# Kernel optimization log

Hardware: AMD Instinct MI355X
Metric: run time of the kernel (lower is better)

Reference implementation:

```python
import math
import jax, jax.numpy as jnp
import numpy as np

DIM = 1024
N_HEADS = 16
N_KV_HEADS = 4
HEAD_DIM = 64
WINDOW = 512
EPS = 1e-6
B, S = 2, 2048

def _alibi_slopes(n_heads):
    def pow2(n):
        r = 2.0 ** (-8.0 / n)
        return np.array([r ** (i + 1) for i in range(n)], dtype=np.float32)
    if math.log2(n_heads).is_integer():
        return pow2(n_heads)
    m = 2 ** math.floor(math.log2(n_heads))
    return np.concatenate([pow2(m), pow2(2 * m)[::2][: n_heads - m]])

def _rmsnorm(x, w, eps=EPS):
    var = jnp.mean(x * x, axis=-1, keepdims=True)
    return x * jax.lax.rsqrt(var + eps) * w

def setup_inputs() -> dict:
    key = jax.random.key(0)
    ks = jax.random.split(key, 8)
    x = jax.random.normal(ks[0], (B, S, DIM), dtype=jnp.float32)
    wq = 0.02 * jax.random.normal(ks[1], (N_HEADS * HEAD_DIM, DIM), dtype=jnp.float32)
    wk = 0.02 * jax.random.normal(ks[2], (N_KV_HEADS * HEAD_DIM, DIM), dtype=jnp.float32)
    wv = 0.02 * jax.random.normal(ks[3], (N_KV_HEADS * HEAD_DIM, DIM), dtype=jnp.float32)
    wo = 0.02 * jax.random.normal(ks[4], (DIM, N_HEADS * HEAD_DIM), dtype=jnp.float32)
    q_norm_w = jnp.ones((N_HEADS * HEAD_DIM,), dtype=jnp.float32)
    k_norm_w = jnp.ones((N_KV_HEADS * HEAD_DIM,), dtype=jnp.float32)
    return {"x": x, "wq": wq, "wk": wk, "wv": wv, "wo": wo,
            "q_norm_w": q_norm_w, "k_norm_w": k_norm_w}

def reference(x, wq, wk, wv, wo, q_norm_w, k_norm_w):
    bsz, seqlen, _ = x.shape
    repeats = N_HEADS // N_KV_HEADS
    xq = _rmsnorm(x @ wq.T, q_norm_w)
    xk = _rmsnorm(x @ wk.T, k_norm_w)
    xv = x @ wv.T
    # [b, h, s, d]
    q = xq.reshape(bsz, seqlen, N_HEADS, HEAD_DIM).transpose(0, 2, 1, 3)
    k = xk.reshape(bsz, seqlen, N_KV_HEADS, HEAD_DIM).transpose(0, 2, 1, 3)
    v = xv.reshape(bsz, seqlen, N_KV_HEADS, HEAD_DIM).transpose(0, 2, 1, 3)
    k = jnp.repeat(k, repeats, axis=1)
    v = jnp.repeat(v, repeats, axis=1)
    pos = jnp.arange(seqlen)
    rel = pos[None, :] - pos[:, None]  # [s_q, s_k], key - query
    slopes = jnp.asarray(_alibi_slopes(N_HEADS))
    bias = slopes[:, None, None] * rel[None].astype(x.dtype)  # [h, s, s]
    masked = (rel > 0) | (rel < -WINDOW)  # causal + sliding window
    bias = jnp.where(masked[None], -jnp.inf, bias)
    scale = 1.0 / math.sqrt(HEAD_DIM)
    scores = jnp.einsum('bhqd,bhkd->bhqk', q, k) * scale + bias[None]
    probs = jax.nn.softmax(scores, axis=-1)
    y = jnp.einsum('bhqk,bhkd->bhqd', probs, v)
    y = y.transpose(0, 2, 1, 3).reshape(bsz, seqlen, N_HEADS * HEAD_DIM)
    return y @ wo.T
```

## Files before the change

kernel.cpp:

```cpp
#include <hip/hip_runtime.h>

typedef unsigned short u16;
typedef unsigned int u32;

typedef __bf16 bf16x8 __attribute__((ext_vector_type(8)));
typedef float f32x4 __attribute__((ext_vector_type(4)));

__device__ __forceinline__ u16 f2bf(float f) {
  u32 u = __builtin_bit_cast(u32, f);
  u32 r = (u + 0x7fffu + ((u >> 16) & 1u)) >> 16;
  return (u16)r;
}
__device__ __forceinline__ float bf2f(u16 v) {
  u32 u = (u32)v << 16;
  return __builtin_bit_cast(float, u);
}

__global__ __launch_bounds__(256)
void cvt_all_kernel(const float* __restrict__ x, const float* __restrict__ wq,
                    const float* __restrict__ wk, const float* __restrict__ wv,
                    const float* __restrict__ wo, u16* __restrict__ x_bf,
                    u16* __restrict__ wcat_bf, u16* __restrict__ wo_bf) {
  int t = blockIdx.x * 256 + threadIdx.x;
  const float* src;
  u16* dst;
  if (t < 1048576) {
    src = x; dst = x_bf;
  } else if (t < 1310720) {
    src = wq; dst = wcat_bf; t -= 1048576;
  } else if (t < 1376256) {
    src = wk; dst = wcat_bf + 1048576; t -= 1310720;
  } else if (t < 1441792) {
    src = wv; dst = wcat_bf + 1310720; t -= 1376256;
  } else {
    src = wo; dst = wo_bf; t -= 1441792;
  }
  const int i = t * 4;
  float4 v = *(const float4*)(src + i);
  uint2 p;
  p.x = (u32)f2bf(v.x) | ((u32)f2bf(v.y) << 16);
  p.y = (u32)f2bf(v.z) | ((u32)f2bf(v.w) << 16);
  *(uint2*)(dst + i) = p;
}

template <typename OutT>
__global__ __launch_bounds__(256)
void gemm_bt_kernel(const u16* __restrict__ A, const u16* __restrict__ B,
                    OutT* __restrict__ C, int M, int N, int K) {
  __shared__ u16 As[64 * 32];
  __shared__ u16 Bs[128 * 32];
  const int tid = threadIdx.x;
  const int lane = tid & 63;
  const int wave = tid >> 6;
  const int wm = (wave >> 1) * 32;
  const int wn = (wave & 1) * 64;
  const int l15 = lane & 15;
  const int qk = (lane >> 4) * 8;
  const size_t bm = (size_t)blockIdx.y * 64;
  const size_t bn = (size_t)blockIdx.x * 128;

  f32x4 acc[2][4];
#pragma unroll
  for (int i = 0; i < 2; ++i)
#pragma unroll
    for (int j = 0; j < 4; ++j) acc[i][j] = f32x4{0.f, 0.f, 0.f, 0.f};

  const int r0 = tid >> 2;
  const int c0 = (tid & 3) * 8;
  const u16* Ab = A + (bm + r0) * (size_t)K + c0;
  const u16* Bb = B + (bn + r0) * (size_t)K + c0;

  uint4 ar = *(const uint4*)(Ab);
  uint4 br0 = *(const uint4*)(Bb);
  uint4 br1 = *(const uint4*)(Bb + (size_t)64 * K);

  for (int k0 = 0; k0 < K; k0 += 32) {
    __syncthreads();
    *(uint4*)(&As[tid * 8]) = ar;
    *(uint4*)(&Bs[tid * 8]) = br0;
    *(uint4*)(&Bs[tid * 8 + 2048]) = br1;
    __syncthreads();
    const int kn = (k0 + 32 < K) ? k0 + 32 : 0;
    ar = *(const uint4*)(Ab + kn);
    br0 = *(const uint4*)(Bb + kn);
    br1 = *(const uint4*)(Bb + (size_t)64 * K + kn);
    bf16x8 af[2], bfr[4];
#pragma unroll
    for (int i = 0; i < 2; ++i)
      af[i] = *(const bf16x8*)(&As[(wm + i * 16 + l15) * 32 + qk]);
#pragma unroll
    for (int j = 0; j < 4; ++j)
      bfr[j] = *(const bf16x8*)(&Bs[(wn + j * 16 + l15) * 32 + qk]);
#pragma unroll
    for (int i = 0; i < 2; ++i)
#pragma unroll
      for (int j = 0; j < 4; ++j)
        acc[i][j] = __builtin_amdgcn_mfma_f32_16x16x32_bf16(af[i], bfr[j], acc[i][j], 0, 0, 0);
  }

  const int rq = (lane >> 4) * 4;
#pragma unroll
  for (int i = 0; i < 2; ++i) {
#pragma unroll
    for (int r = 0; r < 4; ++r) {
      OutT* crow = C + (bm + wm + i * 16 + rq + r) * (size_t)N + bn + wn + l15;
#pragma unroll
      for (int j = 0; j < 4; ++j) {
        if constexpr (sizeof(OutT) == 2)
          crow[j * 16] = f2bf(acc[i][j][r]);
        else
          crow[j * 16] = acc[i][j][r];
      }
    }
  }
}

__global__ __launch_bounds__(256)
void norm_vtrans_kernel(u16* __restrict__ qkv, const float* __restrict__ qw,
                        const float* __restrict__ kw, u16* __restrict__ vt) {
  __shared__ u16 shmem[64 * 72];
  const int bid = blockIdx.x;
  const int tid = threadIdx.x;
  if (bid < 4096) {
    float* red = (float*)shmem;
    u16* row = qkv + (size_t)bid * 1536;
    uint2 pk = *(const uint2*)(row + tid * 4);
    float v0 = bf2f((u16)pk.x), v1 = bf2f((u16)(pk.x >> 16));
    float v2 = bf2f((u16)pk.y), v3 = bf2f((u16)(pk.y >> 16));
    float ss = v0 * v0 + v1 * v1 + v2 * v2 + v3 * v3;
#pragma unroll
    for (int off = 32; off > 0; off >>= 1) ss += __shfl_down(ss, off);
    if ((tid & 63) == 0) red[tid >> 6] = ss;
    __syncthreads();
    float tot = red[0] + red[1] + red[2] + red[3];
    float rn = rsqrtf(tot * (1.0f / 1024.0f) + 1e-6f);
    float4 w = *(const float4*)(qw + tid * 4);
    uint2 po;
    po.x = (u32)f2bf(v0 * rn * w.x) | ((u32)f2bf(v1 * rn * w.y) << 16);
    po.y = (u32)f2bf(v2 * rn * w.z) | ((u32)f2bf(v3 * rn * w.w) << 16);
    *(uint2*)(row + tid * 4) = po;
    if (tid < 64) {
      uint2 kp = *(const uint2*)(row + 1024 + tid * 4);
      float k0 = bf2f((u16)kp.x), k1 = bf2f((u16)(kp.x >> 16));
      float k2 = bf2f((u16)kp.y), k3 = bf2f((u16)(kp.y >> 16));
      float sk = k0 * k0 + k1 * k1 + k2 * k2 + k3 * k3;
#pragma unroll
      for (int off = 32; off > 0; off >>= 1) sk += __shfl_down(sk, off);
      float tk = __shfl(sk, 0);
      float rk = rsqrtf(tk * (1.0f / 256.0f) + 1e-6f);
      float4 w2 = *(const float4*)(kw + tid * 4);
      uint2 ko;
      ko.x = (u32)f2bf(k0 * rk * w2.x) | ((u32)f2bf(k1 * rk * w2.y) << 16);
      ko.y = (u32)f2bf(k2 * rk * w2.z) | ((u32)f2bf(k3 * rk * w2.w) << 16);
      *(uint2*)(row + 1024 + tid * 4) = ko;
    }
  } else {
    const int e = bid - 4096;
    const int t0 = (e & 31) * 64, kvh = (e >> 5) & 3, b = e >> 7;
    u16(*tile)[72] = (u16(*)[72])shmem;
    const int r = tid >> 2, c16 = (tid & 3) * 16;
    const u16* src = qkv + (size_t)(b * 2048 + t0 + r) * 1536 + 1280 + kvh * 64 + c16;
    *(uint4*)&tile[r][c16] = *(const uint4*)src;
    *(uint4*)&tile[r][c16 + 8] = *(const uint4*)(src + 8);
    __syncthreads();
    const int d = tid >> 2, t16 = (tid & 3) * 16;
    u16 o[16];
#pragma unroll
    for (int j = 0; j < 16; ++j) o[j] = tile[t16 + j][d];
    u16* dst = vt + (size_t)((b * 4 + kvh) * 64 + d) * 2048 + t0 + t16;
    *(uint4*)dst = *(uint4*)&o[0];
    *(uint4*)(dst + 8) = *(uint4*)&o[8];
  }
}

__global__ __launch_bounds__(256)
void attn_kernel(const u16* __restrict__ qkvbf, const u16* __restrict__ vt,
                 u16* __restrict__ ybf) {
  __shared__ u16 Ks[64 * 72];
  __shared__ u16 Vts[64 * 72];
  __shared__ u16 Ps[64 * 72];
  const int qt = blockIdx.x, h = blockIdx.y, b = blockIdx.z;
  const int kvh = h >> 2, q0 = qt * 64;
  const int tid = threadIdx.x, lane = tid & 63, w = tid >> 6;
  const int l15 = lane & 15, quad = lane >> 4;

  const u16* qrow = qkvbf + (size_t)(b * 2048 + q0 + w * 16 + l15) * 1536 + h * 64 + quad * 8;
  const bf16x8 qf0 = *(const bf16x8*)qrow;
  const bf16x8 qf1 = *(const bf16x8*)(qrow + 32);

  const int sr = tid >> 2, sc = (tid & 3) * 16;
  const u16* kbase = qkvbf + (size_t)(b * 2048 + sr) * 1536 + 1024 + kvh * 64 + sc;
  const u16* vbase = vt + (size_t)((b * 4 + kvh) * 64 + sr) * 2048 + sc;

  f32x4 O[4];
#pragma unroll
  for (int jd = 0; jd < 4; ++jd) O[jd] = f32x4{0.f, 0.f, 0.f, 0.f};
  float m_i = -1e30f, l_i = 0.f;
  const float LOG2E = 1.44269504f;
  const float sc2 = 0.125f * LOG2E;
  const float slope2 = exp2f(-0.5f * (float)(h + 1)) * LOG2E;
  const int c_lo = (q0 >= 512) ? (q0 - 512) : 0;
  const int myq = q0 + w * 16 + l15;
  const int myq_lo = q0 + w * 16;

  uint4 kr0, kr1, vr0, vr1;
  {
    const u16* kp = kbase + (size_t)c_lo * 1536;
    const u16* vp = vbase + c_lo;
    kr0 = *(const uint4*)kp;  kr1 = *(const uint4*)(kp + 8);
    vr0 = *(const uint4*)vp;  vr1 = *(const uint4*)(vp + 8);
  }

  for (int c = c_lo; c <= q0; c += 64) {
    __syncthreads();
    *(uint4*)&Ks[sr * 72 + sc] = kr0;
    *(uint4*)&Ks[sr * 72 + sc + 8] = kr1;
    *(uint4*)&Vts[sr * 72 + sc] = vr0;
    *(uint4*)&Vts[sr * 72 + sc + 8] = vr1;
    __syncthreads();
    {
      const int cn = (c + 64 <= q0) ? c + 64 : c_lo;
      const u16* kp = kbase + (size_t)cn * 1536;
      const u16* vp = vbase + cn;
      kr0 = *(const uint4*)kp;  kr1 = *(const uint4*)(kp + 8);
      vr0 = *(const uint4*)vp;  vr1 = *(const uint4*)(vp + 8);
    }

    f32x4 st[4];
#pragma unroll
    for (int i = 0; i < 4; ++i) {
      bf16x8 a0 = *(const bf16x8*)&Ks[(i * 16 + l15) * 72 + quad * 8];
      bf16x8 a1 = *(const bf16x8*)&Ks[(i * 16 + l15) * 72 + 32 + quad * 8];
      f32x4 z = f32x4{0.f, 0.f, 0.f, 0.f};
      z = __builtin_amdgcn_mfma_f32_16x16x32_bf16(a0, qf0, z, 0, 0, 0);
      st[i] = __builtin_amdgcn_mfma_f32_16x16x32_bf16(a1, qf1, z, 0, 0, 0);
    }

    float sv[4][4];
    float rm = -1e30f;
    const bool interior = (c + 63 <= myq_lo) && (c + 512 >= myq_lo + 15);
    if (interior) {
#pragma unroll
      for (int i = 0; i < 4; ++i)
#pragma unroll
        for (int r = 0; r < 4; ++r) {
          const int key = c + i * 16 + quad * 4 + r;
          float val = st[i][r] * sc2 + slope2 * (float)(key - myq);
          sv[i][r] = val;
          rm = fmaxf(rm, val);
        }
    } else {
#pragma unroll
      for (int i = 0; i < 4; ++i)
#pragma unroll
        for (int r = 0; r < 4; ++r) {
          const int key = c + i * 16 + quad * 4 + r;
          const int rel = key - myq;
          float val = (rel > 0 || rel < -512) ? -1e30f
                                              : st[i][r] * sc2 + slope2 * (float)rel;
          sv[i][r] = val;
          rm = fmaxf(rm, val);
        }
    }
    rm = fmaxf(rm, __shfl_xor(rm, 16));
    rm = fmaxf(rm, __shfl_xor(rm, 32));
    const float mn = fmaxf(m_i, rm);
    const float alpha = exp2f(m_i - mn);
    float ls = 0.f;
#pragma unroll
    for (int i = 0; i < 4; ++i) {
      float p0 = exp2f(sv[i][0] - mn);
      float p1 = exp2f(sv[i][1] - mn);
      float p2 = exp2f(sv[i][2] - mn);
      float p3 = exp2f(sv[i][3] - mn);
      ls += (p0 + p1) + (p2 + p3);
      uint2 pw;
      pw.x = (u32)f2bf(p0) | ((u32)f2bf(p1) << 16);
      pw.y = (u32)f2bf(p2) | ((u32)f2bf(p3) << 16);
      *(uint2*)&Ps[(w * 16 + l15) * 72 + i * 16 + quad * 4] = pw;
    }
    ls += __shfl_xor(ls, 16);
    ls += __shfl_xor(ls, 32);
    l_i = l_i * alpha + ls;
    m_i = mn;

    float ar[4];
#pragma unroll
    for (int r = 0; r < 4; ++r) ar[r] = __shfl(alpha, quad * 4 + r);
#pragma unroll
    for (int jd = 0; jd < 4; ++jd)
#pragma unroll
      for (int r = 0; r < 4; ++r) O[jd][r] *= ar[r];

    bf16x8 pf0 = *(const bf16x8*)&Ps[(w * 16 + l15) * 72 + quad * 8];
    bf16x8 pf1 = *(const bf16x8*)&Ps[(w * 16 + l15) * 72 + 32 + quad * 8];
#pragma unroll
    for (int jd = 0; jd < 4; ++jd) {
      bf16x8 v0 = *(const bf16x8*)&Vts[(jd * 16 + l15) * 72 + quad * 8];
      bf16x8 v1 = *(const bf16x8*)&Vts[(jd * 16 + l15) * 72 + 32 + quad * 8];
      O[jd] = __builtin_amdgcn_mfma_f32_16x16x32_bf16(pf0, v0, O[jd], 0, 0, 0);
      O[jd] = __builtin_amdgcn_mfma_f32_16x16x32_bf16(pf1, v1, O[jd], 0, 0, 0);
    }
  }

  float lr[4];
#pragma unroll
  for (int r = 0; r < 4; ++r) lr[r] = __shfl(l_i, quad * 4 + r);
#pragma unroll
  for (int r = 0; r < 4; ++r) {
    const float inv = 1.0f / lr[r];
    u16* orow = ybf + (size_t)(b * 2048 + q0 + w * 16 + quad * 4 + r) * 1024 + h * 64 + l15;
#pragma unroll
    for (int jd = 0; jd < 4; ++jd) orow[jd * 16] = f2bf(O[jd][r] * inv);
  }
}

extern "C" void kernel_launch(void* const* d_in, const int* in_sizes, int n_in,
                              void* d_out, int out_size, void* d_ws, size_t ws_size,
                              hipStream_t stream) {
  const float* x = (const float*)d_in[0];
  const float* wq = (const float*)d_in[1];
  const float* wk = (const float*)d_in[2];
  const float* wv = (const float*)d_in[3];
  const float* wo = (const float*)d_in[4];
  const float* qnw = (const float*)d_in[5];
  const float* knw = (const float*)d_in[6];
  float* out = (float*)d_out;
  char* ws = (char*)d_ws;

  u16* x_bf = (u16*)(ws);
  u16* wcat_bf = (u16*)(ws + 8388608);
  u16* wo_bf = (u16*)(ws + 11534336);
  u16* qkv_bf = (u16*)(ws + 13631488);
  u16* vt_bf = (u16*)(ws + 26214400);
  u16* y_bf = (u16*)(ws + 28311552);

  cvt_all_kernel<<<6656, 256, 0, stream>>>(x, wq, wk, wv, wo, x_bf, wcat_bf, wo_bf);

  gemm_bt_kernel<u16><<<dim3(12, 64), 256, 0, stream>>>(x_bf, wcat_bf, qkv_bf, 4096, 1536, 1024);
  norm_vtrans_kernel<<<4352, 256, 0, stream>>>(qkv_bf, qnw, knw, vt_bf);
  attn_kernel<<<dim3(32, 16, 2), 256, 0, stream>>>(qkv_bf, vt_bf, y_bf);
  gemm_bt_kernel<float><<<dim3(8, 64), 256, 0, stream>>>(y_bf, wo_bf, out, 4096, 1024, 1024);
}
```

Baseline: 171.9 us.

## Double attention query tile to 128 rows with 8 waves sharing K/V tiles

Each attention block now handles 128 queries with 512 threads (8 waves) instead of 64 queries with 256 threads, so every K/V tile staged in shared memory serves twice as many queries. Each thread loads one 16-byte chunk of K and V per tile instead of two. Waves whose query range does not overlap the current key tile skip the compute. This halves global K/V traffic per query but causes idle waves at the window edges and halves the grid to 512 blocks, which may reduce occupancy and load balance.

```diff
diff --git a/kernel.cpp b/kernel.cpp
--- a/kernel.cpp
+++ b/kernel.cpp
@@ -173,14 +173,14 @@
   }
 }
 
-__global__ __launch_bounds__(256)
+__global__ __launch_bounds__(512)
 void attn_kernel(const u16* __restrict__ qkvbf, const u16* __restrict__ vt,
                  u16* __restrict__ ybf) {
   __shared__ u16 Ks[64 * 72];
   __shared__ u16 Vts[64 * 72];
-  __shared__ u16 Ps[64 * 72];
+  __shared__ u16 Ps[128 * 72];
   const int qt = blockIdx.x, h = blockIdx.y, b = blockIdx.z;
-  const int kvh = h >> 2, q0 = qt * 64;
+  const int kvh = h >> 2, q0 = qt * 128;
   const int tid = threadIdx.x, lane = tid & 63, w = tid >> 6;
   const int l15 = lane & 15, quad = lane >> 4;
 
@@ -188,7 +188,7 @@
   const bf16x8 qf0 = *(const bf16x8*)qrow;
   const bf16x8 qf1 = *(const bf16x8*)(qrow + 32);
 
-  const int sr = tid >> 2, sc = (tid & 3) * 16;
+  const int sr = tid >> 3, sc = (tid & 7) * 8;
   const u16* kbase = qkvbf + (size_t)(b * 2048 + sr) * 1536 + 1024 + kvh * 64 + sc;
   const u16* vbase = vt + (size_t)((b * 4 + kvh) * 64 + sr) * 2048 + sc;
 
@@ -200,31 +200,26 @@
   const float sc2 = 0.125f * LOG2E;
   const float slope2 = exp2f(-0.5f * (float)(h + 1)) * LOG2E;
   const int c_lo = (q0 >= 512) ? (q0 - 512) : 0;
-  const int myq = q0 + w * 16 + l15;
+  const int c_hi = q0 + 64;
   const int myq_lo = q0 + w * 16;
-
-  uint4 kr0, kr1, vr0, vr1;
-  {
-    const u16* kp = kbase + (size_t)c_lo * 1536;
-    const u16* vp = vbase + c_lo;
-    kr0 = *(const uint4*)kp;  kr1 = *(const uint4*)(kp + 8);
-    vr0 = *(const uint4*)vp;  vr1 = *(const uint4*)(vp + 8);
-  }
-
-  for (int c = c_lo; c <= q0; c += 64) {
-    __syncthreads();
-    *(uint4*)&Ks[sr * 72 + sc] = kr0;
-    *(uint4*)&Ks[sr * 72 + sc + 8] = kr1;
-    *(uint4*)&Vts[sr * 72 + sc] = vr0;
-    *(uint4*)&Vts[sr * 72 + sc + 8] = vr1;
+  const int myq_hi = myq_lo + 15;
+  const int myq = myq_lo + l15;
+
+  uint4 kr = *(const uint4*)(kbase + (size_t)c_lo * 1536);
+  uint4 vr = *(const uint4*)(vbase + c_lo);
+
+  for (int c = c_lo; c <= c_hi; c += 64) {
+    __syncthreads();
+    *(uint4*)&Ks[sr * 72 + sc] = kr;
+    *(uint4*)&Vts[sr * 72 + sc] = vr;
     __syncthreads();
     {
-      const int cn = (c + 64 <= q0) ? c + 64 : c_lo;
-      const u16* kp = kbase + (size_t)cn * 1536;
-      const u16* vp = vbase + cn;
-      kr0 = *(const uint4*)kp;  kr1 = *(const uint4*)(kp + 8);
-      vr0 = *(const uint4*)vp;  vr1 = *(const uint4*)(vp + 8);
-    }
+      const int cn = (c + 64 <= c_hi) ? c + 64 : c_lo;
+      kr = *(const uint4*)(kbase + (size_t)cn * 1536);
+      vr = *(const uint4*)(vbase + cn);
+    }
+
+    if (c > myq_hi || c + 63 < myq_lo - 512) continue;
 
     f32x4 st[4];
 #pragma unroll
@@ -238,7 +233,7 @@
 
     float sv[4][4];
     float rm = -1e30f;
-    const bool interior = (c + 63 <= myq_lo) && (c + 512 >= myq_lo + 15);
+    const bool interior = (c + 63 <= myq_lo) && (c + 512 >= myq_hi);
     if (interior) {
 #pragma unroll
       for (int i = 0; i < 4; ++i)
@@ -339,6 +334,6 @@
 
   gemm_bt_kernel<u16><<<dim3(12, 64), 256, 0, stream>>>(x_bf, wcat_bf, qkv_bf, 4096, 1536, 1024);
   norm_vtrans_kernel<<<4352, 256, 0, stream>>>(qkv_bf, qnw, knw, vt_bf);
-  attn_kernel<<<dim3(32, 16, 2), 256, 0, stream>>>(qkv_bf, vt_bf, y_bf);
+  attn_kernel<<<dim3(16, 16, 2), 512, 0, stream>>>(qkv_bf, vt_bf, y_bf);
   gemm_bt_kernel<float><<<dim3(8, 64), 256, 0, stream>>>(y_bf, wo_bf, out, 4096, 1024, 1024);
 }
```

Result: no change. 170.0 us (-1.1%).
